# Kernel optimization log

Measured on AMD Instinct MI355X. Metric: run time of the kernel, lower is better.

The kernel has to match this reference:

```python
import jax, jax.numpy as jnp
import numpy as np
import math

NUM_HEADS = 16
D_EMBED = 1024
D_HEAD = D_EMBED // NUM_HEADS


def setup_inputs() -> dict:
    key = jax.random.key(0)
    k1, k2, k3 = jax.random.split(key, 3)
    B, S = 4, 2048
    x = jax.random.normal(k1, (B, S, D_EMBED), dtype=jnp.float32)
    # Kaiming-ish init for the fused QKV and output projections
    scale_in = 1.0 / math.sqrt(D_EMBED)
    in_proj_weight = jax.random.normal(k2, (3 * D_EMBED, D_EMBED), dtype=jnp.float32) * scale_in
    out_proj_weight = jax.random.normal(k3, (D_EMBED, D_EMBED), dtype=jnp.float32) * scale_in
    return {
        "x": x,
        "in_proj_weight": in_proj_weight,
        "out_proj_weight": out_proj_weight,
        "causal_mask": 1,
    }


def reference(x, in_proj_weight, out_proj_weight, causal_mask):
    B, S, D = x.shape
    # fused QKV projection: x @ W_in^T -> [B, S, 3D], then split
    qkv = jnp.einsum("bsd,ed->bse", x, in_proj_weight)
    q, k, v = jnp.split(qkv, 3, axis=-1)
    # [B, S, H, dh] -> [B, H, S, dh]
    def to_heads(t):
        return t.reshape(B, S, NUM_HEADS, D_HEAD).transpose(0, 2, 1, 3)
    q, k, v = to_heads(q), to_heads(k), to_heads(v)
    # scores: [B, H, S, S]
    scores = jnp.einsum("bhqd,bhkd->bhqk", q, k) / math.sqrt(D_HEAD)
    if causal_mask:
        mask = jnp.triu(jnp.ones((S, S), dtype=bool), k=1)
        scores = jnp.where(mask, -jnp.inf, scores)
    attn = jax.nn.softmax(scores, axis=-1)
    out = jnp.einsum("bhqk,bhkd->bhqd", attn, v)
    out = out.transpose(0, 2, 1, 3).reshape(B, S, D)
    return jnp.einsum("bsd,ed->bse", out, out_proj_weight)
```

## Files before the change

### kernel.cpp

```cpp
#include <hip/hip_runtime.h>
#include <hip/hip_bf16.h>
#include <stdint.h>

typedef unsigned short u16;
typedef __attribute__((ext_vector_type(8))) short short8;
typedef __attribute__((ext_vector_type(4))) float floatx4;
typedef __attribute__((ext_vector_type(16))) float floatx16;
typedef __attribute__((ext_vector_type(4))) unsigned uint4v;
typedef __attribute__((ext_vector_type(2))) unsigned uint2v;

#define DEV static __device__ __forceinline__

DEV u16 f2bf(float f) {
  __hip_bfloat16 h = __float2bfloat16(f);
  return __builtin_bit_cast(u16, h);
}

DEV float fexp2(float x) {
  float r;
  asm("v_exp_f32 %0, %1" : "=v"(r) : "v"(x));
  return r;
}

DEV unsigned cvtpk(float lo, float hi) {
  unsigned r;
  asm("v_cvt_pk_bf16_f32 %0, %1, %2" : "=v"(r) : "v"(lo), "v"(hi));
  return r;
}

DEV void pswap(unsigned& a, unsigned& b) {
  uint2v r = __builtin_amdgcn_permlane32_swap(a, b, false, false);
  a = r[0];
  b = r[1];
}

DEV void cross32(float v, float& x, float& y) {
  unsigned a = __builtin_bit_cast(unsigned, v), b = a;
  pswap(a, b);
  x = __builtin_bit_cast(float, a);
  y = __builtin_bit_cast(float, b);
}

DEV floatx4 mfma16(short8 a, short8 b, floatx4 c) {
  return __builtin_amdgcn_mfma_f32_16x16x32_bf16(a, b, c, 0, 0, 0);
}
DEV floatx16 mfma32(short8 a, short8 b, floatx16 c) {
  return __builtin_amdgcn_mfma_f32_32x32x16_bf16(a, b, c, 0, 0, 0);
}

DEV void gload_lds16(const void* g, void* l) {
  __builtin_amdgcn_global_load_lds(
      (void __attribute__((address_space(1)))*)(g),
      (void __attribute__((address_space(3)))*)(l),
      16, 0, 0);
}

__global__ void cast_kernel(const float* __restrict__ in, u16* __restrict__ out, int n4) {
  int i = blockIdx.x * 256 + threadIdx.x;
  if (i >= n4) return;
  float4 v = reinterpret_cast<const float4*>(in)[i];
  ushort4 o;
  o.x = f2bf(v.x); o.y = f2bf(v.y); o.z = f2bf(v.z); o.w = f2bf(v.w);
  reinterpret_cast<ushort4*>(out)[i] = o;
}

template <int MODE>
__global__ __launch_bounds__(256, 2)
void gemm_bt(const u16* __restrict__ A, const u16* __restrict__ W,
             int M, int N, int K,
             u16* __restrict__ Qb, u16* __restrict__ Kb, u16* __restrict__ Vb,
             float* __restrict__ C) {
  __shared__ u16 As[2][128 * 32];
  __shared__ u16 Bs[2][128 * 32];
  const int tid = threadIdx.x;
  const int wave = tid >> 6, lane = tid & 63;
  const int lr = lane & 15, lg = lane >> 4;
  const int m0 = blockIdx.y * 128, n0 = blockIdx.x * 128;
  const int mq0 = (wave >> 1) * 64, nq0 = (wave & 1) * 64;
  const int srow = lane >> 2;
  const int sk8  = (lane & 3) * 8;

  floatx4 acc[4][4];
#pragma unroll
  for (int i = 0; i < 4; ++i)
#pragma unroll
    for (int j = 0; j < 4; ++j) acc[i][j] = (floatx4)0.f;

#pragma unroll
  for (int i = 0; i < 2; ++i) {
    int seg = wave + 4 * i;
    int r = seg * 16 + srow;
    gload_lds16(&A[(size_t)(m0 + r) * K + sk8], &As[0][seg * 512]);
    gload_lds16(&W[(size_t)(n0 + r) * K + sk8], &Bs[0][seg * 512]);
  }
  __syncthreads();

  int cur = 0;
  for (int kt = 0; kt < K; kt += 32) {
    if (kt + 32 < K) {
#pragma unroll
      for (int i = 0; i < 2; ++i) {
        int seg = wave + 4 * i;
        int r = seg * 16 + srow;
        gload_lds16(&A[(size_t)(m0 + r) * K + kt + 32 + sk8], &As[cur ^ 1][seg * 512]);
        gload_lds16(&W[(size_t)(n0 + r) * K + kt + 32 + sk8], &Bs[cur ^ 1][seg * 512]);
      }
    }

    short8 af[4], bf[4];
#pragma unroll
    for (int t = 0; t < 4; ++t)
      af[t] = *reinterpret_cast<const short8*>(&As[cur][(mq0 + t * 16 + lr) * 32 + lg * 8]);
#pragma unroll
    for (int t = 0; t < 4; ++t)
      bf[t] = *reinterpret_cast<const short8*>(&Bs[cur][(nq0 + t * 16 + lr) * 32 + lg * 8]);
#pragma unroll
    for (int i = 0; i < 4; ++i)
#pragma unroll
      for (int j = 0; j < 4; ++j)
        acc[i][j] = mfma16(af[i], bf[j], acc[i][j]);

    __syncthreads();
    cur ^= 1;
  }

  if (MODE == 0) {
#pragma unroll
    for (int j = 0; j < 4; ++j) {
      int n = n0 + nq0 + j * 16 + lr;
      int which = n >> 10;
      int d = n & 1023;
      int h = d >> 6, dh = d & 63;
      u16* dst = (which == 0) ? Qb : ((which == 1) ? Kb : Vb);
      float scale = (which == 0) ? 0.18033688f : 1.0f;
#pragma unroll
      for (int i = 0; i < 4; ++i) {
#pragma unroll
        for (int r = 0; r < 4; ++r) {
          int m = m0 + mq0 + i * 16 + lg * 4 + r;
          int b = m >> 11, s = m & 2047;
          dst[((size_t)(b * 16 + h) * 2048 + s) * 64 + dh] = f2bf(acc[i][j][r] * scale);
        }
      }
    }
  } else {
#pragma unroll
    for (int i = 0; i < 4; ++i)
#pragma unroll
      for (int j = 0; j < 4; ++j)
#pragma unroll
        for (int r = 0; r < 4; ++r) {
          int m = m0 + mq0 + i * 16 + lg * 4 + r;
          int n = n0 + nq0 + j * 16 + lr;
          C[(size_t)m * N + n] = acc[i][j][r];
        }
  }
}

__global__ __launch_bounds__(256, 2)
void attn_kernel(const u16* __restrict__ Qb, const u16* __restrict__ Kb,
                 const u16* __restrict__ Vb, u16* __restrict__ Ob) {
  const int bh = blockIdx.y;
  const u16* Qh = Qb + (size_t)bh * 2048 * 64;
  const u16* Kh = Kb + (size_t)bh * 2048 * 64;
  const u16* Vh = Vb + (size_t)bh * 2048 * 64;

  __shared__ u16 smem[3][8192];

  const int tid = threadIdx.x, wave = tid >> 6, lane = tid & 63;
  const int ln31 = lane & 31, hi = lane >> 5;
  const int swz = (lane & 7) * 8;
  const int b = bh >> 4, h = bh & 15;

  const int vp = tid & 31, vc8 = tid >> 5;

  auto stage_k = [&](int kvbase, u16* buf) {
#pragma unroll
    for (int i = 0; i < 2; ++i) {
      int s = i * 256 + tid;
      int row = s >> 3;
      int col = ((s & 7) ^ (row & 7)) * 8;
      gload_lds16(&Kh[(size_t)(kvbase + row) * 64 + col], &buf[(size_t)s * 8]);
    }
  };
  auto load_v = [&](int kvbase, short8& v0, short8& v1) {
    v0 = *reinterpret_cast<const short8*>(&Vh[(size_t)(kvbase + 2 * vp) * 64 + vc8 * 8]);
    v1 = *reinterpret_cast<const short8*>(&Vh[(size_t)(kvbase + 2 * vp + 1) * 64 + vc8 * 8]);
  };
  auto write_v = [&](u16* buf, short8 v0, short8 v1) {
#pragma unroll
    for (int j = 0; j < 8; ++j) {
      int d = vc8 * 8 + j;
      uint32_t pk = (uint32_t)(u16)v0[j] | ((uint32_t)(u16)v1[j] << 16);
      *reinterpret_cast<uint32_t*>(&buf[4096 + d * 64 + ((2 * vp) ^ ((d & 7) * 8))]) = pk;
    }
  };

  for (int ph = 0; ph < 2; ++ph) {
    const int tq = ph ? (15 - (int)blockIdx.x) : (int)blockIdx.x;
    const int q0w = tq * 128 + wave * 32;
    const int qrow = q0w + ln31;

    short8 qf[4];
#pragma unroll
    for (int c = 0; c < 4; ++c)
      qf[c] = *reinterpret_cast<const short8*>(
          &Qh[(size_t)qrow * 64 + c * 16 + hi * 8]);

    floatx16 accO0 = (floatx16)0.f, accO1 = (floatx16)0.f;
    float m_run = -1e30f, l_run = 0.f;

    auto do_qk = [&](int kvq, floatx16& SQ0, floatx16& SQ1, const u16* Ksq) {
      if (kvq > q0w + 31) return;
      SQ0 = (floatx16)0.f;
      SQ1 = (floatx16)0.f;
      __builtin_amdgcn_s_setprio(1);
#pragma unroll
      for (int c = 0; c < 4; ++c) {
        short8 kfA = *reinterpret_cast<const short8*>(
            &Ksq[ln31 * 64 + ((c * 16 + hi * 8) ^ swz)]);
        short8 kfB = *reinterpret_cast<const short8*>(
            &Ksq[(32 + ln31) * 64 + ((c * 16 + hi * 8) ^ swz)]);
        SQ0 = mfma32(kfA, qf[c], SQ0);
        SQ1 = mfma32(kfB, qf[c], SQ1);
      }
      __builtin_amdgcn_s_setprio(0);
    };

    auto do_smpv = [&](int kv0_, floatx16& SS0, floatx16& SS1, const u16* bufv) {
      if (kv0_ > q0w + 31) return;
      if (kv0_ + 63 > q0w) {
#pragma unroll
        for (int reg = 0; reg < 16; ++reg) {
          int kvA = kv0_ + (reg & 3) + 8 * (reg >> 2) + 4 * hi;
          if (kvA > qrow) SS0[reg] = -1e30f;
          if (kvA + 32 > qrow) SS1[reg] = -1e30f;
        }
      }
      float m8[8];
#pragma unroll
      for (int i = 0; i < 8; ++i)
        m8[i] = fmaxf(fmaxf(SS0[i], SS0[i + 8]), fmaxf(SS1[i], SS1[i + 8]));
      float mx = fmaxf(fmaxf(fmaxf(m8[0], m8[1]), fmaxf(m8[2], m8[3])),
                       fmaxf(fmaxf(m8[4], m8[5]), fmaxf(m8[6], m8[7])));
      {
        float xa, xb;
        cross32(mx, xa, xb);
        mx = fmaxf(xa, xb);
      }
      bool small_ = (mx <= m_run + 8.f);
      if (!__all(small_)) {
        float mn = fmaxf(m_run, mx);
        float fac = fexp2(m_run - mn);
        m_run = mn;
        l_run *= fac;
        accO0 *= fac;
        accO1 *= fac;
      }
#pragma unroll
      for (int i = 0; i < 16; ++i) SS0[i] = fexp2(SS0[i] - m_run);
#pragma unroll
      for (int i = 0; i < 16; ++i) SS1[i] = fexp2(SS1[i] - m_run);
      float a8[8];
#pragma unroll
      for (int i = 0; i < 8; ++i)
        a8[i] = (SS0[i] + SS0[i + 8]) + (SS1[i] + SS1[i + 8]);
      float rs = ((a8[0] + a8[1]) + (a8[2] + a8[3])) + ((a8[4] + a8[5]) + (a8[6] + a8[7]));
      {
        float xa, xb;
        cross32(rs, xa, xb);
        rs = xa + xb;
      }
      l_run += rs;
      short8 pf[4];
#define BUILD_PF(idx, S, base)                                        \
      {                                                               \
        unsigned u01 = cvtpk(S[base + 0], S[base + 1]);               \
        unsigned u23 = cvtpk(S[base + 2], S[base + 3]);               \
        unsigned u45 = cvtpk(S[base + 4], S[base + 5]);               \
        unsigned u67 = cvtpk(S[base + 6], S[base + 7]);               \
        pswap(u01, u45);                                              \
        pswap(u23, u67);                                              \
        uint4v w; w.x = u01; w.y = u23; w.z = u45; w.w = u67;         \
        pf[idx] = __builtin_bit_cast(short8, w);                      \
      }
      BUILD_PF(0, SS0, 0)
      BUILD_PF(1, SS0, 8)
      BUILD_PF(2, SS1, 0)
      BUILD_PF(3, SS1, 8)
#undef BUILD_PF
      const u16* Vt = bufv + 4096;
      __builtin_amdgcn_s_setprio(1);
#pragma unroll
      for (int c = 0; c < 4; ++c) {
        short8 vfA = *reinterpret_cast<const short8*>(
            &Vt[ln31 * 64 + ((c * 16 + hi * 8) ^ swz)]);
        short8 vfB = *reinterpret_cast<const short8*>(
            &Vt[(32 + ln31) * 64 + ((c * 16 + hi * 8) ^ swz)]);
        accO0 = mfma32(vfA, pf[c], accO0);
        accO1 = mfma32(vfB, pf[c], accO1);
      }
      __builtin_amdgcn_s_setprio(0);
    };

    const int nt = 2 * (tq + 1);

    __syncthreads();
    stage_k(0, smem[0]);
    {
      short8 v0, v1;
      load_v(0, v0, v1);
      write_v(smem[0], v0, v1);
    }
    stage_k(64, smem[1]);
    {
      short8 v0, v1;
      load_v(64, v0, v1);
      write_v(smem[1], v0, v1);
    }
    __syncthreads();

    floatx16 SA0, SA1, SB0, SB1;
    do_qk(0, SA0, SA1, smem[0]);

    for (int it = 0; it < nt; it += 2) {
      {
        const int kvc = it * 64;
        short8 nv0, nv1;
        const bool do_st = (it + 2) < nt;
        u16* sbuf = smem[(it + 2) % 3];
        if (do_st) {
          stage_k(kvc + 128, sbuf);
          load_v(kvc + 128, nv0, nv1);
        }
        do_qk(kvc + 64, SB0, SB1, smem[(it + 1) % 3]);
        do_smpv(kvc, SA0, SA1, smem[it % 3]);
        if (do_st) write_v(sbuf, nv0, nv1);
        __syncthreads();
      }
      {
        const int kvc = it * 64 + 64;
        short8 nv0, nv1;
        const bool do_st = (it + 3) < nt;
        u16* sbuf = smem[(it + 3) % 3];
        if (do_st) {
          stage_k(kvc + 128, sbuf);
          load_v(kvc + 128, nv0, nv1);
        }
        if (it + 2 < nt) do_qk(kvc + 64, SA0, SA1, smem[(it + 2) % 3]);
        do_smpv(kvc, SB0, SB1, smem[(it + 1) % 3]);
        if (do_st) write_v(sbuf, nv0, nv1);
        __syncthreads();
      }
    }

    u16* ep = &smem[0][0] + wave * 2048;
    float inv = 1.0f / l_run;
#define EPI_W(ACC, dh2)                                               \
    {                                                                 \
      _Pragma("unroll")                                               \
      for (int rp = 0; rp < 8; ++rp) {                                \
        int reg = rp * 2;                                             \
        unsigned pk = cvtpk(ACC[reg] * inv, ACC[reg + 1] * inv);      \
        int d = dh2 * 32 + (reg & 3) + 8 * (reg >> 2) + 4 * hi;       \
        *reinterpret_cast<uint32_t*>(                                 \
            &ep[ln31 * 64 + (d ^ ((ln31 & 7) * 8))]) = pk;            \
      }                                                               \
    }
    EPI_W(accO0, 0)
    EPI_W(accO1, 1)
#undef EPI_W
#pragma unroll
    for (int g = 0; g < 4; ++g) {
      int d0 = hi * 32 + g * 8;
      short8 o8 = *reinterpret_cast<const short8*>(
          &ep[ln31 * 64 + (d0 ^ ((ln31 & 7) * 8))]);
      *reinterpret_cast<short8*>(
          &Ob[(size_t)(b * 2048 + q0w + ln31) * 1024 + h * 64 + d0]) = o8;
    }
  }
}

extern "C" void kernel_launch(void* const* d_in, const int* in_sizes, int n_in,
                              void* d_out, int out_size, void* d_ws, size_t ws_size,
                              hipStream_t stream) {
  const float* x    = (const float*)d_in[0];
  const float* win  = (const float*)d_in[1];
  const float* wout = (const float*)d_in[2];
  float* out = (float*)d_out;

  char* ws = (char*)d_ws;
  u16* xb    = (u16*)(ws + 0);
  u16* winb  = (u16*)(ws + 16777216);
  u16* woutb = (u16*)(ws + 23068672);
  u16* Qb    = (u16*)(ws + 25165824);
  u16* Kb    = (u16*)(ws + 41943040);
  u16* Vb    = (u16*)(ws + 58720256);
  u16* Ob    = (u16*)(ws + 75497472);

  cast_kernel<<<8192, 256, 0, stream>>>(x, xb, 2097152);
  cast_kernel<<<3072, 256, 0, stream>>>(win, winb, 786432);
  cast_kernel<<<1024, 256, 0, stream>>>(wout, woutb, 262144);

  gemm_bt<0><<<dim3(24, 64), 256, 0, stream>>>(xb, winb, 8192, 3072, 1024,
                                               Qb, Kb, Vb, nullptr);
  attn_kernel<<<dim3(8, 64), 256, 0, stream>>>(Qb, Kb, Vb, Ob);
  gemm_bt<1><<<dim3(8, 64), 256, 0, stream>>>(Ob, woutb, 8192, 1024, 1024,
                                              nullptr, nullptr, nullptr, out);
}
```

Before: 182.4 us.

## Triple-buffer GEMM LDS pipeline with swizzle, single barrier; merge cast kernels

```diff
diff --git a/kernel.cpp b/kernel.cpp
--- a/kernel.cpp
+++ b/kernel.cpp
@@ -55,13 +55,25 @@
       16, 0, 0);
 }
 
-__global__ void cast_kernel(const float* __restrict__ in, u16* __restrict__ out, int n4) {
+__global__ void cast3_kernel(const float* __restrict__ x, const float* __restrict__ win,
+                             const float* __restrict__ wout,
+                             u16* __restrict__ xb, u16* __restrict__ winb,
+                             u16* __restrict__ woutb) {
   int i = blockIdx.x * 256 + threadIdx.x;
-  if (i >= n4) return;
-  float4 v = reinterpret_cast<const float4*>(in)[i];
+  const float* src;
+  u16* dst;
+  int off;
+  if (i < 2097152) {
+    src = x; dst = xb; off = i;
+  } else if (i < 2883584) {
+    src = win; dst = winb; off = i - 2097152;
+  } else {
+    src = wout; dst = woutb; off = i - 2883584;
+  }
+  float4 v = reinterpret_cast<const float4*>(src)[off];
   ushort4 o;
   o.x = f2bf(v.x); o.y = f2bf(v.y); o.z = f2bf(v.z); o.w = f2bf(v.w);
-  reinterpret_cast<ushort4*>(out)[i] = o;
+  reinterpret_cast<ushort4*>(dst)[off] = o;
 }
 
 template <int MODE>
@@ -70,15 +82,16 @@
              int M, int N, int K,
              u16* __restrict__ Qb, u16* __restrict__ Kb, u16* __restrict__ Vb,
              float* __restrict__ C) {
-  __shared__ u16 As[2][128 * 32];
-  __shared__ u16 Bs[2][128 * 32];
+  __shared__ u16 As[3][128 * 32];
+  __shared__ u16 Bs[3][128 * 32];
   const int tid = threadIdx.x;
   const int wave = tid >> 6, lane = tid & 63;
   const int lr = lane & 15, lg = lane >> 4;
   const int m0 = blockIdx.y * 128, n0 = blockIdx.x * 128;
   const int mq0 = (wave >> 1) * 64, nq0 = (wave & 1) * 64;
-  const int srow = lane >> 2;
-  const int sk8  = (lane & 3) * 8;
+  const int scol = ((lane & 3) ^ ((lane >> 3) & 3)) * 8;
+  const int srow_lo = lane >> 2;
+  const int swz2 = ((lr >> 1) & 3) * 8;
 
   floatx4 acc[4][4];
 #pragma unroll
@@ -86,42 +99,56 @@
 #pragma unroll
     for (int j = 0; j < 4; ++j) acc[i][j] = (floatx4)0.f;
 
-#pragma unroll
-  for (int i = 0; i < 2; ++i) {
-    int seg = wave + 4 * i;
-    int r = seg * 16 + srow;
-    gload_lds16(&A[(size_t)(m0 + r) * K + sk8], &As[0][seg * 512]);
-    gload_lds16(&W[(size_t)(n0 + r) * K + sk8], &Bs[0][seg * 512]);
-  }
-  __syncthreads();
-
-  int cur = 0;
-  for (int kt = 0; kt < K; kt += 32) {
-    if (kt + 32 < K) {
-#pragma unroll
-      for (int i = 0; i < 2; ++i) {
-        int seg = wave + 4 * i;
-        int r = seg * 16 + srow;
-        gload_lds16(&A[(size_t)(m0 + r) * K + kt + 32 + sk8], &As[cur ^ 1][seg * 512]);
-        gload_lds16(&W[(size_t)(n0 + r) * K + kt + 32 + sk8], &Bs[cur ^ 1][seg * 512]);
-      }
-    }
+  const int NT = K >> 5;
+
+  auto stage = [&](int t, int bi) {
+#pragma unroll
+    for (int i2 = 0; i2 < 2; ++i2) {
+      int base_row = wave * 16 + i2 * 64;
+      int r = base_row + srow_lo;
+      gload_lds16(&A[(size_t)(m0 + r) * K + t * 32 + scol],
+                  &As[bi][(size_t)(wave * 64 + i2 * 256) * 8]);
+      gload_lds16(&W[(size_t)(n0 + r) * K + t * 32 + scol],
+                  &Bs[bi][(size_t)(wave * 64 + i2 * 256) * 8]);
+    }
+  };
+
+  stage(0, 0);
+  stage(1, 1);
+
+  int bi = 0;
+  for (int t = 0; t < NT; ++t) {
+    if (t < NT - 1) {
+      asm volatile("s_waitcnt vmcnt(4)" ::: "memory");
+    } else {
+      asm volatile("s_waitcnt vmcnt(0)" ::: "memory");
+    }
+    __builtin_amdgcn_sched_barrier(0);
+    __builtin_amdgcn_s_barrier();
+    __builtin_amdgcn_sched_barrier(0);
+
+    int b2 = bi + 2; if (b2 >= 3) b2 -= 3;
+    if (t + 2 < NT) stage(t + 2, b2);
 
     short8 af[4], bf[4];
 #pragma unroll
-    for (int t = 0; t < 4; ++t)
-      af[t] = *reinterpret_cast<const short8*>(&As[cur][(mq0 + t * 16 + lr) * 32 + lg * 8]);
-#pragma unroll
-    for (int t = 0; t < 4; ++t)
-      bf[t] = *reinterpret_cast<const short8*>(&Bs[cur][(nq0 + t * 16 + lr) * 32 + lg * 8]);
+    for (int m = 0; m < 4; ++m)
+      af[m] = *reinterpret_cast<const short8*>(
+          &As[bi][(mq0 + m * 16 + lr) * 32 + (lg * 8 ^ swz2)]);
+#pragma unroll
+    for (int nn = 0; nn < 4; ++nn)
+      bf[nn] = *reinterpret_cast<const short8*>(
+          &Bs[bi][(nq0 + nn * 16 + lr) * 32 + (lg * 8 ^ swz2)]);
+
+    __builtin_amdgcn_s_setprio(1);
 #pragma unroll
     for (int i = 0; i < 4; ++i)
 #pragma unroll
       for (int j = 0; j < 4; ++j)
         acc[i][j] = mfma16(af[i], bf[j], acc[i][j]);
-
-    __syncthreads();
-    cur ^= 1;
+    __builtin_amdgcn_s_setprio(0);
+
+    if (++bi == 3) bi = 0;
   }
 
   if (MODE == 0) {
@@ -398,9 +425,7 @@
   u16* Vb    = (u16*)(ws + 58720256);
   u16* Ob    = (u16*)(ws + 75497472);
 
-  cast_kernel<<<8192, 256, 0, stream>>>(x, xb, 2097152);
-  cast_kernel<<<3072, 256, 0, stream>>>(win, winb, 786432);
-  cast_kernel<<<1024, 256, 0, stream>>>(wout, woutb, 262144);
+  cast3_kernel<<<12288, 256, 0, stream>>>(x, win, wout, xb, winb, woutb);
 
   gemm_bt<0><<<dim3(24, 64), 256, 0, stream>>>(xb, winb, 8192, 3072, 1024,
                                                Qb, Kb, Vb, nullptr);
```

Measured after the change: 173.5 us. 4.9% less time.
